# Optimization experiments

Hardware: AMD Instinct MI355X
Metric: run time of the kernel (lower is better)

Reference implementation:

```python
import jax, jax.numpy as jnp
import numpy as np

HEADS = 16
S = 1024      # affine_dim
B, L = 4, 2048


def _conv1x1(x, W, b):
    # Conv1d with kernel_size=1: pointwise channel mixing. x: (B, C, L)
    return jnp.einsum('oc,bcl->bol', W, x) + b[None, :, None]


def setup_inputs() -> dict:
    key = jax.random.key(0)
    ks = jax.random.split(key, 7)
    scale = 1.0 / np.sqrt(S)  # ~ torch Conv1d default init scale
    return {
        'x':  jax.random.normal(ks[0], (B, S, L), dtype=jnp.float32),
        'Wk': jax.random.normal(ks[1], (S, S), dtype=jnp.float32) * scale,
        'bk': jax.random.normal(ks[2], (S,), dtype=jnp.float32) * scale,
        'Wq': jax.random.normal(ks[3], (S, S), dtype=jnp.float32) * scale,
        'bq': jax.random.normal(ks[4], (S,), dtype=jnp.float32) * scale,
        'Wp': jax.random.normal(ks[5], (S, S), dtype=jnp.float32) * scale,
        'bp': jax.random.normal(ks[6], (S,), dtype=jnp.float32) * scale,
    }


def reference(x, Wk, bk, Wq, bq, Wp, bp):
    b, c, l = x.shape
    h = HEADS
    d = c // h
    keys = _conv1x1(x, Wk, bk).reshape(b, h, d, l)
    queries = _conv1x1(x, Wq, bq).reshape(b, h, d, l)
    # scores[b,h,i,j] = sum_d keys[...,d,i] * queries[...,d,j]  (keys^T @ queries)
    # NOTE: original scales by `seqlen ** 1 / 2` == seqlen / 2 (Python precedence),
    # i.e. multiply by 2/L, NOT 1/sqrt(L). Faithfully preserved.
    scores = jnp.einsum('bhdi,bhdj->bhij', keys, queries) * (2.0 / l)
    attn = jax.nn.softmax(scores, axis=-1)
    xh = x.reshape(b, h, d, l)  # raw x used as values
    out = jnp.einsum('bhdi,bhij->bhdj', xh, attn).reshape(b, c, l)
    return _conv1x1(out, Wp, bp)
```

## Files before the change

### kernel.cpp

```cpp
#include <hip/hip_runtime.h>
#include <hip/hip_bf16.h>
#include <cstdint>
#include <cstddef>

#ifndef __has_builtin
#define __has_builtin(x) 0
#endif

#define DEVI __device__ __forceinline__

typedef __attribute__((ext_vector_type(8))) __bf16 bf16x8;
typedef __attribute__((ext_vector_type(4))) float float4v;
typedef __attribute__((ext_vector_type(16))) float float16v;
typedef __attribute__((ext_vector_type(4))) unsigned short ushort4v;
typedef __attribute__((ext_vector_type(4))) unsigned int uint4v;

constexpr int Bd = 4, Sd = 1024, Ld = 2048, Hd = 16, Dd = 64;

DEVI unsigned short f2bf(float x){
  union { float f; unsigned u; } v; v.f = x;
  unsigned r = v.u + 0x7fffu + ((v.u >> 16) & 1u);
  return (unsigned short)(r >> 16);
}

DEVI unsigned pack2(float lo, float hi){
  return (unsigned)f2bf(lo) | ((unsigned)f2bf(hi) << 16);
}

DEVI float fast_exp2(float x){
#if __has_builtin(__builtin_amdgcn_exp2f)
  return __builtin_amdgcn_exp2f(x);
#else
  return exp2f(x);
#endif
}

DEVI void plane32_swap(unsigned &a, unsigned &b){
  asm("v_permlane32_swap_b32 %0, %1" : "+v"(a), "+v"(b));
}

DEVI void gload_lds16(const void* g, void* lds){
  __builtin_amdgcn_global_load_lds(
      (const __attribute__((address_space(1))) void*)g,
      (__attribute__((address_space(3))) void*)lds,
      16, 0, 0);
}

DEVI float4v mfma_bf16(bf16x8 a, bf16x8 b, float4v c){
  return __builtin_amdgcn_mfma_f32_16x16x32_bf16(a, b, c, 0, 0, 0);
}

DEVI float16v mfma32_bf16(bf16x8 a, bf16x8 b, float16v c){
  return __builtin_amdgcn_mfma_f32_32x32x16_bf16(a, b, c, 0, 0, 0);
}


__global__ void wcast_kernel(const float* __restrict__ Wk, const float* __restrict__ Wq,
                             const float* __restrict__ Wp,
                             unsigned short* __restrict__ Wkbf, unsigned short* __restrict__ Wqbf,
                             unsigned short* __restrict__ Wpbf, float ck){
  size_t i = ((size_t)blockIdx.x * 256 + threadIdx.x) * 4;
  float4v a = *(const float4v*)(Wk + i);
  float4v b = *(const float4v*)(Wq + i);
  float4v c = *(const float4v*)(Wp + i);
  ushort4v oa = { f2bf(a[0]*ck), f2bf(a[1]*ck), f2bf(a[2]*ck), f2bf(a[3]*ck) };
  ushort4v ob = { f2bf(b[0]), f2bf(b[1]), f2bf(b[2]), f2bf(b[3]) };
  ushort4v oc = { f2bf(c[0]), f2bf(c[1]), f2bf(c[2]), f2bf(c[3]) };
  *(ushort4v*)(Wkbf + i) = oa;
  *(ushort4v*)(Wqbf + i) = ob;
  *(ushort4v*)(Wpbf + i) = oc;
}

__global__ void transpose_cast(const float* __restrict__ x, unsigned short* __restrict__ Xt){
  __shared__ float tile[32][33];
  const int b = blockIdx.z;
  const int l0 = blockIdx.x * 32;
  const int s0 = blockIdx.y * 32;
  const int tx = threadIdx.x, ty = threadIdx.y;
  #pragma unroll
  for (int r = 0; r < 32; r += 8)
    tile[ty + r][tx] = x[((size_t)b*Sd + s0 + ty + r)*Ld + l0 + tx];
  __syncthreads();
  #pragma unroll
  for (int r = 0; r < 32; r += 8)
    Xt[((size_t)b*Ld + l0 + ty + r)*Sd + s0 + tx] = f2bf(tile[tx][ty + r]);
}

__global__ void vprime_kernel(const float* __restrict__ x, const float* __restrict__ invZ,
                              unsigned short* __restrict__ Vp){
  size_t idx = ((size_t)blockIdx.x * 256 + threadIdx.x) * 4;
  const int l = (int)(idx & (Ld - 1));
  const int c = (int)((idx >> 11) & (Sd - 1));
  const int b = (int)(idx >> 21);
  const int h = c >> 6;
  float4v xv = *(const float4v*)(x + idx);
  float4v zv = *(const float4v*)(invZ + ((size_t)(b*Hd + h) * Ld + l));
  ushort4v o = { f2bf(xv[0]*zv[0]), f2bf(xv[1]*zv[1]), f2bf(xv[2]*zv[2]), f2bf(xv[3]*zv[3]) };
  *(ushort4v*)(Vp + idx) = o;
}

template<int OUT_MODE>
__global__ __launch_bounds__(256, 2)
void conv_gemm(const unsigned short* __restrict__ A,
               const unsigned short* __restrict__ Bt,
               const float* __restrict__ bias, float bscale,
               unsigned short* __restrict__ outT,
               float* __restrict__ outF)
{
  constexpr int BK = 32;
  constexpr int NKSTEP = Sd / BK;
  __shared__ __attribute__((aligned(16))) unsigned short Abuf[2][128*BK];
  __shared__ __attribute__((aligned(16))) unsigned short Bbuf[2][128*BK];

  const int b  = blockIdx.z;
  const int n0 = blockIdx.x * 128;
  const int m0 = blockIdx.y * 128;
  const int tid = threadIdx.x;
  const int w = tid >> 6, lane = tid & 63, lr = lane & 15, lg = lane >> 4;
  const int wm = (w >> 1) * 64, wn = (w & 1) * 64;

  const unsigned short* Abase = A + (size_t)m0 * Sd;
  const unsigned short* Bbase = Bt + ((size_t)b * Ld + n0) * Sd;

  auto stage = [&](int bf, int kt){
    #pragma unroll
    for (int p = 0; p < 2; ++p){
      int slot = p*256 + tid;
      int row = slot >> 2, c = slot & 3;
      int csrc = c ^ ((row >> 1) & 3);
      gload_lds16(Abase + (size_t)row * Sd + kt*BK + csrc*8,
                  (void*)(&Abuf[bf][(size_t)(p*256 + w*64) * 8]));
    }
    #pragma unroll
    for (int p = 0; p < 2; ++p){
      int slot = p*256 + tid;
      int row = slot >> 2, c = slot & 3;
      int csrc = c ^ ((row >> 1) & 3);
      gload_lds16(Bbase + (size_t)row * Sd + kt*BK + csrc*8,
                  (void*)(&Bbuf[bf][(size_t)(p*256 + w*64) * 8]));
    }
  };

  const int gsw = lg ^ ((lr >> 1) & 3);

  float4v acc[4][4];
  #pragma unroll
  for (int i = 0; i < 4; ++i)
    #pragma unroll
    for (int j = 0; j < 4; ++j)
      acc[i][j] = (float4v){0.f, 0.f, 0.f, 0.f};

  stage(0, 0);
  __syncthreads();
  int cur = 0;
  for (int kt = 0; kt < NKSTEP; ++kt){
    if (kt + 1 < NKSTEP) stage(cur ^ 1, kt + 1);
    bf16x8 af[4], bfv[4];
    #pragma unroll
    for (int i = 0; i < 4; ++i){
      int row = wm + i*16 + lr;
      af[i] = *(const bf16x8*)((const char*)&Abuf[cur][0] + (size_t)row*64 + gsw*16);
    }
    #pragma unroll
    for (int j = 0; j < 4; ++j){
      int row = wn + j*16 + lr;
      bfv[j] = *(const bf16x8*)((const char*)&Bbuf[cur][0] + (size_t)row*64 + gsw*16);
    }
    #pragma unroll
    for (int i = 0; i < 4; ++i)
      #pragma unroll
      for (int j = 0; j < 4; ++j)
        acc[i][j] = mfma_bf16(af[i], bfv[j], acc[i][j]);
    __syncthreads();
    cur ^= 1;
  }

  #pragma unroll
  for (int i = 0; i < 4; ++i){
    const int mb = m0 + wm + i*16 + lg*4;
    float4v bv = *(const float4v*)(bias + mb);
    #pragma unroll
    for (int j = 0; j < 4; ++j){
      const int n = n0 + wn + j*16 + lr;
      float4v v = acc[i][j];
      float o0 = v[0] + bscale*bv[0];
      float o1 = v[1] + bscale*bv[1];
      float o2 = v[2] + bscale*bv[2];
      float o3 = v[3] + bscale*bv[3];
      if (OUT_MODE == 0){
        ushort4v o = { f2bf(o0), f2bf(o1), f2bf(o2), f2bf(o3) };
        *(ushort4v*)(outT + ((size_t)b*Ld + n)*Sd + mb) = o;
      } else {
        outF[((size_t)b*Sd + mb + 0)*Ld + n] = o0;
        outF[((size_t)b*Sd + mb + 1)*Ld + n] = o1;
        outF[((size_t)b*Sd + mb + 2)*Ld + n] = o2;
        outF[((size_t)b*Sd + mb + 3)*Ld + n] = o3;
      }
    }
  }
}

__global__ __launch_bounds__(256, 2)
void stats_kernel(const unsigned short* __restrict__ Kt,
                  const unsigned short* __restrict__ Qt,
                  float* __restrict__ invZ)
{
  const int bh = blockIdx.y, b = bh >> 4, h = bh & 15;
  const int i0 = blockIdx.x * 64;
  const int tid = threadIdx.x, w = tid >> 6, lane = tid & 63, lr = lane & 15, lg = lane >> 4;

  bf16x8 ka[4][2];
  #pragma unroll
  for (int is = 0; is < 4; ++is)
    #pragma unroll
    for (int ks = 0; ks < 2; ++ks)
      ka[is][ks] = *(const bf16x8*)(Kt + ((size_t)b*Ld + i0 + is*16 + lr)*Sd + h*64 + lg*8 + ks*32);

  float z[4][4] = {};
  for (int js = 0; js < 32; ++js){
    const int jw = js*64 + w*16;
    bf16x8 qb[2];
    #pragma unroll
    for (int ks = 0; ks < 2; ++ks)
      qb[ks] = *(const bf16x8*)(Qt + ((size_t)b*Ld + jw + lr)*Sd + h*64 + lg*8 + ks*32);
    #pragma unroll
    for (int is = 0; is < 4; ++is){
      float4v acc = {0.f, 0.f, 0.f, 0.f};
      acc = mfma_bf16(ka[is][0], qb[0], acc);
      acc = mfma_bf16(ka[is][1], qb[1], acc);
      #pragma unroll
      for (int r = 0; r < 4; ++r) z[is][r] += fast_exp2(acc[r]);
    }
  }
  #pragma unroll
  for (int is = 0; is < 4; ++is)
    #pragma unroll
    for (int r = 0; r < 4; ++r){
      float v = z[is][r];
      #pragma unroll
      for (int m = 1; m < 16; m <<= 1) v += __shfl_xor(v, m, 64);
      z[is][r] = v;
    }
  __shared__ float zred[4][64];
  if (lr == 0){
    #pragma unroll
    for (int is = 0; is < 4; ++is)
      #pragma unroll
      for (int r = 0; r < 4; ++r)
        zred[w][is*16 + lg*4 + r] = z[is][r];
  }
  __syncthreads();
  if (tid < 64){
    float zt = zred[0][tid] + zred[1][tid] + zred[2][tid] + zred[3][tid];
    invZ[(size_t)bh * Ld + i0 + tid] = 1.0f / zt;
  }
}

__global__ __launch_bounds__(256, 4)
void attn_pv_kernel(const unsigned short* __restrict__ Kt,
                    const unsigned short* __restrict__ Qt,
                    const unsigned short* __restrict__ Vp,
                    unsigned short* __restrict__ AOt)
{
  __shared__ __attribute__((aligned(16))) unsigned short Kbuf[2][64*64];
  __shared__ __attribute__((aligned(16))) unsigned short Vbuf[2][64*64];

  const int m = blockIdx.x;
  const int xcd = m & 7, slot = m >> 3;
  const int bh = xcd * 8 + (slot >> 4);
  const int jb = slot & 15;
  const int b = bh >> 4, h = bh & 15;
  const int j0 = jb * 128;

  const int tid = threadIdx.x, w = tid >> 6, lane = tid & 63;
  const int l31 = lane & 31, lh = lane >> 5;
  const int jw = j0 + w * 32;

  bf16x8 qb[4];
  #pragma unroll
  for (int ks = 0; ks < 4; ++ks)
    qb[ks] = *(const bf16x8*)(Qt + ((size_t)b*Ld + jw + l31)*Sd + h*64 + ks*16 + lh*8);

  float16v oacc[2];
  #pragma unroll
  for (int ds = 0; ds < 2; ++ds)
    #pragma unroll
    for (int r = 0; r < 16; ++r) oacc[ds][r] = 0.f;

  const size_t kbase = (size_t)b*Ld*Sd + (size_t)h*64;
  const size_t vbase = ((size_t)b*Sd + h*64)*Ld;

  auto stage = [&](int bf, int it){
    const int i0 = it * 64;
    #pragma unroll
    for (int p = 0; p < 2; ++p){
      const int slot2 = p*256 + tid;
      const int row = slot2 >> 3;
      const int gsrc = (slot2 & 7) ^ (row & 7);
      gload_lds16(Kt + kbase + (size_t)(i0 + row)*Sd + gsrc*8,
                  (void*)(&Kbuf[bf][(size_t)slot2 * 8]));
      gload_lds16(Vp + vbase + (size_t)row*Ld + i0 + gsrc*8,
                  (void*)(&Vbuf[bf][(size_t)slot2 * 8]));
    }
  };

  stage(0, 0);
  __syncthreads();
  int cur = 0;
  for (int it = 0; it < 32; ++it){
    if (it + 1 < 32) stage(cur ^ 1, it + 1);

    float16v sacc[2];
    #pragma unroll
    for (int is = 0; is < 2; ++is){
      #pragma unroll
      for (int r = 0; r < 16; ++r) sacc[is][r] = 0.f;
      #pragma unroll
      for (int ks = 0; ks < 4; ++ks){
        const int row = is*32 + l31;
        const int g = (2*ks + lh) ^ (l31 & 7);
        bf16x8 kf = *(const bf16x8*)((const char*)&Kbuf[cur][0] + (size_t)row*128 + g*16);
        sacc[is] = mfma32_bf16(kf, qb[ks], sacc[is]);
      }
    }

    bf16x8 pf[4];
    #pragma unroll
    for (int is = 0; is < 2; ++is){
      #pragma unroll
      for (int hs = 0; hs < 2; ++hs){
        const int r0 = 8*hs;
        unsigned W0 = pack2(fast_exp2(sacc[is][r0+0]), fast_exp2(sacc[is][r0+1]));
        unsigned W1 = pack2(fast_exp2(sacc[is][r0+2]), fast_exp2(sacc[is][r0+3]));
        unsigned W2 = pack2(fast_exp2(sacc[is][r0+4]), fast_exp2(sacc[is][r0+5]));
        unsigned W3 = pack2(fast_exp2(sacc[is][r0+6]), fast_exp2(sacc[is][r0+7]));
        plane32_swap(W0, W2);
        plane32_swap(W1, W3);
        union { uint4v u; bf16x8 v; } cvt;
        cvt.u = (uint4v){ W0, W1, W2, W3 };
        pf[is*2 + hs] = cvt.v;
      }
    }

    #pragma unroll
    for (int kp = 0; kp < 4; ++kp){
      #pragma unroll
      for (int ds = 0; ds < 2; ++ds){
        const int row = ds*32 + l31;
        const int g = (2*kp + lh) ^ (l31 & 7);
        bf16x8 vf = *(const bf16x8*)((const char*)&Vbuf[cur][0] + (size_t)row*128 + g*16);
        oacc[ds] = mfma32_bf16(vf, pf[kp], oacc[ds]);
      }
    }

    __syncthreads();
    cur ^= 1;
  }

  #pragma unroll
  for (int ds = 0; ds < 2; ++ds){
    #pragma unroll
    for (int rq = 0; rq < 4; ++rq){
      const int d0 = ds*32 + 8*rq + 4*lh;
      ushort4v o = { f2bf(oacc[ds][4*rq+0]), f2bf(oacc[ds][4*rq+1]),
                     f2bf(oacc[ds][4*rq+2]), f2bf(oacc[ds][4*rq+3]) };
      *(ushort4v*)(AOt + ((size_t)b*Ld + jw + l31)*Sd + h*64 + d0) = o;
    }
  }
}


extern "C" void kernel_launch(void* const* d_in, const int* in_sizes, int n_in,
                              void* d_out, int out_size, void* d_ws, size_t ws_size,
                              hipStream_t stream)
{
  const float* x  = (const float*)d_in[0];
  const float* Wk = (const float*)d_in[1];
  const float* bk = (const float*)d_in[2];
  const float* Wq = (const float*)d_in[3];
  const float* bq = (const float*)d_in[4];
  const float* Wp = (const float*)d_in[5];
  const float* bp = (const float*)d_in[6];
  float* out = (float*)d_out;

  char* ws = (char*)d_ws;
  const size_t SZ_BLS = (size_t)Bd * Ld * Sd * 2;
  unsigned short* Xt   = (unsigned short*)(ws);
  unsigned short* Kt   = (unsigned short*)(ws + SZ_BLS);
  unsigned short* Qt   = (unsigned short*)(ws + 2*SZ_BLS);
  unsigned short* AOt  = (unsigned short*)(ws + 3*SZ_BLS);
  unsigned short* Wkbf = (unsigned short*)(ws + 4*SZ_BLS);
  unsigned short* Wqbf = (unsigned short*)(ws + 4*SZ_BLS + (size_t)2097152);
  unsigned short* Wpbf = (unsigned short*)(ws + 4*SZ_BLS + (size_t)2*2097152);
  float* invZ          = (float*)(ws + 4*SZ_BLS + (size_t)3*2097152);
  unsigned short* Vp   = Xt;

  const float ck = (2.0f / (float)Ld) * 1.44269504088896f;

  wcast_kernel<<<1024, 256, 0, stream>>>(Wk, Wq, Wp, Wkbf, Wqbf, Wpbf, ck);
  transpose_cast<<<dim3(Ld/32, Sd/32, Bd), dim3(32, 8), 0, stream>>>(x, Xt);

  dim3 cg(Ld/128, Sd/128, Bd);
  conv_gemm<0><<<cg, 256, 0, stream>>>(Wkbf, Xt, bk, ck,   Kt, nullptr);
  conv_gemm<0><<<cg, 256, 0, stream>>>(Wqbf, Xt, bq, 1.0f, Qt, nullptr);

  stats_kernel<<<dim3(Ld/64, Bd*Hd), 256, 0, stream>>>(Kt, Qt, invZ);
  vprime_kernel<<<(Bd*(size_t)Sd*Ld/4)/256, 256, 0, stream>>>(x, invZ, Vp);
  attn_pv_kernel<<<dim3((Ld/128)*(Bd*Hd)), 256, 0, stream>>>(Kt, Qt, Vp, AOt);

  conv_gemm<1><<<cg, 256, 0, stream>>>(Wpbf, AOt, bp, 1.0f, nullptr, out);
}
```

Measured before the change: 257.8 us.

## Restructure softmax stats kernel with LDS-staged Q tiles and 32x32 MFMA

The row-sum (softmax denominator) kernel now stages Q tiles into swizzled LDS with double-buffered async global-to-LDS loads, shared by all four waves. Each wave holds a 32-row K fragment and uses 32x32x16 MFMAs, so each lane accumulates one row's sum without the cross-lane shuffle reduction or the LDS reduction at the end. The grid is remapped to 128-row blocks with XCD-aware ordering, and launch bounds are raised to 4 blocks per CU. The bf16 packing helper also uses a byte-permute instruction. This aims to cut redundant global Q reads and reduction overhead, at the cost of LDS use and barriers.

```diff
diff --git a/kernel.cpp b/kernel.cpp
--- a/kernel.cpp
+++ b/kernel.cpp
@@ -24,7 +24,14 @@
 }
 
 DEVI unsigned pack2(float lo, float hi){
-  return (unsigned)f2bf(lo) | ((unsigned)f2bf(hi) << 16);
+  union { float f; unsigned u; } a, b; a.f = lo; b.f = hi;
+  unsigned ra = a.u + 0x7fffu + ((a.u >> 16) & 1u);
+  unsigned rb = b.u + 0x7fffu + ((b.u >> 16) & 1u);
+#if __has_builtin(__builtin_amdgcn_perm)
+  return __builtin_amdgcn_perm(rb, ra, 0x07060302u);
+#else
+  return (ra >> 16) | (rb & 0xffff0000u);
+#endif
 }
 
 DEVI float fast_exp2(float x){
@@ -200,60 +207,70 @@
   }
 }
 
-__global__ __launch_bounds__(256, 2)
+__global__ __launch_bounds__(256, 4)
 void stats_kernel(const unsigned short* __restrict__ Kt,
                   const unsigned short* __restrict__ Qt,
                   float* __restrict__ invZ)
 {
-  const int bh = blockIdx.y, b = bh >> 4, h = bh & 15;
-  const int i0 = blockIdx.x * 64;
-  const int tid = threadIdx.x, w = tid >> 6, lane = tid & 63, lr = lane & 15, lg = lane >> 4;
-
-  bf16x8 ka[4][2];
-  #pragma unroll
-  for (int is = 0; is < 4; ++is)
-    #pragma unroll
-    for (int ks = 0; ks < 2; ++ks)
-      ka[is][ks] = *(const bf16x8*)(Kt + ((size_t)b*Ld + i0 + is*16 + lr)*Sd + h*64 + lg*8 + ks*32);
-
-  float z[4][4] = {};
-  for (int js = 0; js < 32; ++js){
-    const int jw = js*64 + w*16;
-    bf16x8 qb[2];
-    #pragma unroll
-    for (int ks = 0; ks < 2; ++ks)
-      qb[ks] = *(const bf16x8*)(Qt + ((size_t)b*Ld + jw + lr)*Sd + h*64 + lg*8 + ks*32);
-    #pragma unroll
-    for (int is = 0; is < 4; ++is){
-      float4v acc = {0.f, 0.f, 0.f, 0.f};
-      acc = mfma_bf16(ka[is][0], qb[0], acc);
-      acc = mfma_bf16(ka[is][1], qb[1], acc);
-      #pragma unroll
-      for (int r = 0; r < 4; ++r) z[is][r] += fast_exp2(acc[r]);
-    }
+  __shared__ __attribute__((aligned(16))) unsigned short Qbuf[2][64*64];
+
+  const int m = blockIdx.x;
+  const int xcd = m & 7, slot = m >> 3;
+  const int bh = xcd * 8 + (slot >> 4);
+  const int ib = slot & 15;
+  const int b = bh >> 4, h = bh & 15;
+  const int i0 = ib * 128;
+
+  const int tid = threadIdx.x, w = tid >> 6, lane = tid & 63;
+  const int l31 = lane & 31, lh = lane >> 5;
+  const int iw = i0 + w * 32;
+
+  bf16x8 kb[4];
+  #pragma unroll
+  for (int ks = 0; ks < 4; ++ks)
+    kb[ks] = *(const bf16x8*)(Kt + ((size_t)b*Ld + iw + l31)*Sd + h*64 + ks*16 + lh*8);
+
+  const size_t qbase = (size_t)b*Ld*Sd + (size_t)h*64;
+  auto stage = [&](int bf, int jt){
+    const int j0 = jt * 64;
+    #pragma unroll
+    for (int p = 0; p < 2; ++p){
+      const int slot2 = p*256 + tid;
+      const int row = slot2 >> 3;
+      const int gsrc = (slot2 & 7) ^ (row & 7);
+      gload_lds16(Qt + qbase + (size_t)(j0 + row)*Sd + gsrc*8,
+                  (void*)(&Qbuf[bf][(size_t)slot2 * 8]));
+    }
+  };
+
+  float z = 0.f;
+  stage(0, 0);
+  __syncthreads();
+  int cur = 0;
+  for (int jt = 0; jt < 32; ++jt){
+    if (jt + 1 < 32) stage(cur ^ 1, jt + 1);
+    #pragma unroll
+    for (int js = 0; js < 2; ++js){
+      float16v sacc;
+      #pragma unroll
+      for (int r = 0; r < 16; ++r) sacc[r] = 0.f;
+      #pragma unroll
+      for (int ks = 0; ks < 4; ++ks){
+        const int row = js*32 + l31;
+        const int g = (2*ks + lh) ^ (l31 & 7);
+        bf16x8 qf = *(const bf16x8*)((const char*)&Qbuf[cur][0] + (size_t)row*128 + g*16);
+        sacc = mfma32_bf16(qf, kb[ks], sacc);
+      }
+      #pragma unroll
+      for (int r = 0; r < 16; ++r) z += fast_exp2(sacc[r]);
+    }
+    __syncthreads();
+    cur ^= 1;
   }
-  #pragma unroll
-  for (int is = 0; is < 4; ++is)
-    #pragma unroll
-    for (int r = 0; r < 4; ++r){
-      float v = z[is][r];
-      #pragma unroll
-      for (int m = 1; m < 16; m <<= 1) v += __shfl_xor(v, m, 64);
-      z[is][r] = v;
-    }
-  __shared__ float zred[4][64];
-  if (lr == 0){
-    #pragma unroll
-    for (int is = 0; is < 4; ++is)
-      #pragma unroll
-      for (int r = 0; r < 4; ++r)
-        zred[w][is*16 + lg*4 + r] = z[is][r];
-  }
-  __syncthreads();
-  if (tid < 64){
-    float zt = zred[0][tid] + zred[1][tid] + zred[2][tid] + zred[3][tid];
-    invZ[(size_t)bh * Ld + i0 + tid] = 1.0f / zt;
-  }
+
+  z += __shfl_xor(z, 32, 64);
+  if (lh == 0)
+    invZ[(size_t)bh * Ld + iw + l31] = 1.0f / z;
 }
 
 __global__ __launch_bounds__(256, 4)
@@ -404,7 +421,7 @@
   conv_gemm<0><<<cg, 256, 0, stream>>>(Wkbf, Xt, bk, ck,   Kt, nullptr);
   conv_gemm<0><<<cg, 256, 0, stream>>>(Wqbf, Xt, bq, 1.0f, Qt, nullptr);
 
-  stats_kernel<<<dim3(Ld/64, Bd*Hd), 256, 0, stream>>>(Kt, Qt, invZ);
+  stats_kernel<<<dim3((Ld/128)*(Bd*Hd)), 256, 0, stream>>>(Kt, Qt, invZ);
   vprime_kernel<<<(Bd*(size_t)Sd*Ld/4)/256, 256, 0, stream>>>(x, invZ, Vp);
   attn_pv_kernel<<<dim3((Ld/128)*(Bd*Hd)), 256, 0, stream>>>(Kt, Qt, Vp, AOt);
 
```

Result: faster. 235.6 us (-8.6%).
